# Optimization experiments

Hardware: AMD Instinct MI355X
Metric: run time of the kernel (lower is better)

Reference implementation:

```python
import jax, jax.numpy as jnp
import numpy as np

B, N, D, H, K, FFN = 8, 256, 512, 16, 4, 2048
DK = D // H
NEG = -1e12


def _lin(k, i, o):
    return jax.random.normal(k, (i, o), jnp.float32) / np.sqrt(i)


def setup_inputs() -> dict:
    key = jax.random.key(0)
    ks = jax.random.split(key, 12)
    return {
        "x": jax.random.normal(ks[0], (B, N, D), jnp.float32),
        "dist": jax.random.uniform(ks[1], (B, N - 1, N - 1), jnp.float32) * 10.0,
        "dist_bar": jnp.array([1.5, 3.0, 5.0, 8.0], jnp.float32),
        "attn_bias": 0.1 * jax.random.normal(ks[2], (B, K, N, N), jnp.float32),
        "mask": jnp.ones((B, 1, N, N), jnp.int32),
        "num_heads": H,
        "Wq": _lin(ks[3], D, D), "bq": jnp.zeros((D,), jnp.float32),
        "Wk": _lin(ks[4], D, D), "bk": jnp.zeros((D,), jnp.float32),
        "Wv": _lin(ks[5], D, D), "bv": jnp.zeros((D,), jnp.float32),
        "W1": _lin(ks[6], K * D, D), "b1": jnp.zeros((D,), jnp.float32),
        "W2": _lin(ks[7], D, D), "b2": jnp.zeros((D,), jnp.float32),
        "g1": jnp.ones((D,), jnp.float32), "be1": jnp.zeros((D,), jnp.float32),
        "Wf1": _lin(ks[8], D, FFN), "bf1": jnp.zeros((FFN,), jnp.float32),
        "Wf2": _lin(ks[9], FFN, D), "bf2": jnp.zeros((D,), jnp.float32),
        "g2": jnp.ones((D,), jnp.float32), "be2": jnp.zeros((D,), jnp.float32),
    }


def _ln(x, g, b, eps=1e-6):
    m = jnp.mean(x, -1, keepdims=True)
    v = jnp.mean((x - m) ** 2, -1, keepdims=True)
    return (x - m) / jnp.sqrt(v + eps) * g + b


def _forward(x, dist, dist_bar, attn_bias, mask, num_heads,
             Wq, bq, Wk, bk, Wv, bv, W1, b1, W2, b2, g1, be1,
             Wf1, bf1, Wf2, bf2, g2, be2):
    Bn, Nn, Dn = x.shape
    Hh = num_heads
    dk = Dn // Hh
    Kk = dist_bar.shape[0]

    q = (x @ Wq + bq).reshape(Bn, Nn, Hh, dk).transpose(0, 2, 1, 3)  # [B,H,N,dk]
    k = (x @ Wk + bk).reshape(Bn, Nn, Hh, dk).transpose(0, 2, 1, 3)
    v = (x @ Wv + bv).reshape(Bn, Nn, Hh, dk).transpose(0, 2, 1, 3)

    scores = jnp.einsum('bhnd,bhmd->bhnm', q, k) / np.sqrt(dk)      # [B,H,N,N]
    # expand over scales and add bias: [B,H,K,N,N]
    scores = scores[:, :, None, :, :] + attn_bias[:, None, :, :, :]
    # padding mask [B,1,N,N] -> broadcast over H,K
    scores = jnp.where(mask[:, None] == 0, NEG, scores)

    # build padded distance with super node (row/col 0 distance = 0)
    nd = jnp.ones((Bn, Nn, Nn), x.dtype)
    nd = nd.at[:, 1:, 1:].set(dist)
    nd = nd.at[:, 0, :].set(0.0).at[:, :, 0].set(0.0)
    masks = nd[:, None, None, :, :] < dist_bar.reshape(1, 1, Kk, 1, 1)  # [B,1,K,N,N]
    masks = masks.at[:, :, :, 0, :].set(True).at[:, :, :, :, 0].set(True)

    scores = jnp.where(masks, scores, NEG)
    attn = jax.nn.softmax(scores, axis=-1)                           # [B,H,K,N,N]

    msg = jnp.einsum('bhknm,bhmd->bhknd', attn, v)                   # [B,H,K,N,dk]
    # faithful to torch: transpose(1,2).view(B,H*K,N,dk) then transpose(2,3).view(B,N,-1)
    msg = jnp.transpose(msg, (0, 2, 1, 3, 4)).reshape(Bn, Kk * Hh, Nn, dk)
    msg = jnp.transpose(msg, (0, 1, 3, 2)).reshape(Bn, Nn, Kk * Hh * dk)

    h = jax.nn.silu(msg @ W1 + b1) @ W2 + b2
    y = _ln(h + x, g1, be1)

    f = jax.nn.gelu(y @ Wf1 + bf1, approximate=False) @ Wf2 + bf2
    out = _ln(f + y, g2, be2)
    return out


def reference(x, dist, dist_bar, attn_bias, mask, num_heads,
              Wq, bq, Wk, bk, Wv, bv, W1, b1, W2, b2, g1, be1,
              Wf1, bf1, Wf2, bf2, g2, be2):
    return _forward(x, dist, dist_bar, attn_bias, mask, num_heads,
                    Wq, bq, Wk, bk, Wv, bv, W1, b1, W2, b2, g1, be1,
                    Wf1, bf1, Wf2, bf2, g2, be2)
```

## Files before the change

### kernel.cpp

```cpp
#include <hip/hip_runtime.h>
#include <math.h>

#define BB 8
#define NN 256
#define DD 512
#define HH 16
#define KK 4
#define DKK 32
#define FFN_ 2048
#define NEGV -1e12f

typedef __attribute__((ext_vector_type(8))) short bf16x8;
typedef __attribute__((ext_vector_type(4))) float f32x4;

__device__ __forceinline__ unsigned short f2bf(float f) {
    union { float f; unsigned int u; } v; v.f = f;
    unsigned int r = (v.u + 0x7FFFu + ((v.u >> 16) & 1u)) >> 16;
    return (unsigned short)r;
}
__device__ __forceinline__ float bf2f(unsigned short u) {
    union { unsigned int i; float f; } v; v.i = ((unsigned int)u) << 16;
    return v.f;
}
__device__ __forceinline__ void gload_lds16(const unsigned short* g, unsigned short* l) {
    __builtin_amdgcn_global_load_lds(
        (const __attribute__((address_space(1))) void*)g,
        (__attribute__((address_space(3))) void*)l, 16, 0, 0);
}

__global__ __launch_bounds__(256) void prep_kernel(
    const float* __restrict__ x,
    const float* __restrict__ Wq, const float* __restrict__ Wk,
    const float* __restrict__ Wv, const float* __restrict__ W1,
    const float* __restrict__ W2, const float* __restrict__ Wf1,
    const float* __restrict__ Wf2,
    const float* __restrict__ bq, const float* __restrict__ bk,
    const float* __restrict__ bv,
    const float* __restrict__ attn_bias, const int* __restrict__ mask,
    const float* __restrict__ dist, const float* __restrict__ dist_bar,
    unsigned short* __restrict__ xb, unsigned short* __restrict__ Wqkvt,
    unsigned short* __restrict__ W1t, unsigned short* __restrict__ W2t,
    unsigned short* __restrict__ Wf1t, unsigned short* __restrict__ Wf2t,
    float* __restrict__ bqkv, unsigned short* __restrict__ biasMs)
{
    const int z = blockIdx.z;
    const int t = threadIdx.x;

    if (z == 7) {
        if (blockIdx.x >= 1024) return;
        const int i0 = blockIdx.x * 1024 + t * 4;
        float4 xv = *(const float4*)(x + i0);
        ushort4 o;
        o.x = f2bf(xv.x); o.y = f2bf(xv.y); o.z = f2bf(xv.z); o.w = f2bf(xv.w);
        *(ushort4*)(xb + i0) = o;
        return;
    }
    if (z == 8) {
        if (blockIdx.x >= 6) return;
        const int i = blockIdx.x * 256 + t;
        float v = (i < 512) ? bq[i] : (i < 1024) ? bk[i - 512] : bv[i - 1024];
        bqkv[i] = v;
        return;
    }
    if (z == 9) {
        const int bx = blockIdx.x;
        const int rg = bx & 63, ks = (bx >> 6) & 3, b = bx >> 8;
        const int m = t;
        const float bar = dist_bar[ks];
        ushort4 o; unsigned short* po = (unsigned short*)&o;
        #pragma unroll
        for (int i = 0; i < 4; ++i) {
            const int n = rg * 4 + i;
            const int mk = mask[((size_t)(b * NN) + n) * NN + m];
            bool allowed = (n == 0) || (m == 0);
            if (!allowed)
                allowed = dist[((size_t)(b * 255) + (n - 1)) * 255 + (m - 1)] < bar;
            const float bias = attn_bias[(((size_t)(b * KK) + ks) * NN + n) * NN + m];
            po[i] = f2bf((mk != 0 && allowed) ? bias : NEGV);
        }
        *(ushort4*)(biasMs + (size_t)bx * 1024 + m * 4) = o;
        return;
    }

    const float* src; unsigned short* dst; int Kd, Nd;
    switch (z) {
        case 0: src = Wq;  dst = Wqkvt;              Kd = 512;  Nd = 512;  break;
        case 1: src = Wk;  dst = Wqkvt + 512 * 512;  Kd = 512;  Nd = 512;  break;
        case 2: src = Wv;  dst = Wqkvt + 1024 * 512; Kd = 512;  Nd = 512;  break;
        case 3: src = W1;  dst = W1t;  Kd = 2048; Nd = 512;  break;
        case 4: src = W2;  dst = W2t;  Kd = 512;  Nd = 512;  break;
        case 5: src = Wf1; dst = Wf1t; Kd = 512;  Nd = 2048; break;
        default: src = Wf2; dst = Wf2t; Kd = 2048; Nd = 512; break;
    }
    const int ktiles = Kd / 32, ntiles = Nd / 32;
    const int ti = blockIdx.x;
    if (ti >= ktiles * ntiles) return;
    const int k0 = (ti % ktiles) * 32, n0 = (ti / ktiles) * 32;

    __shared__ float tile[32][33];
    const int xx = t & 31, yy = t >> 5;
    #pragma unroll
    for (int r = 0; r < 4; ++r)
        tile[yy * 4 + r][xx] = src[(size_t)(k0 + yy * 4 + r) * Nd + n0 + xx];
    __syncthreads();
    #pragma unroll
    for (int r = 0; r < 4; ++r)
        dst[(size_t)(n0 + yy * 4 + r) * Kd + k0 + xx] = f2bf(tile[xx][yy * 4 + r]);
}

template<int ACT, int EPI>
__global__ __launch_bounds__(512) void mfma_gemm512(
    const unsigned short* __restrict__ A, const unsigned short* __restrict__ Bt,
    const float* __restrict__ bias, unsigned short* __restrict__ Cb,
    unsigned short* __restrict__ vT, int M, int N, int Kdim)
{
    __shared__ unsigned short As[128 * 64];
    __shared__ unsigned short Bs[128 * 64];

    const int t = threadIdx.x, lane = t & 63, wv = t >> 6;
    const int n0 = blockIdx.x * 128, m0 = blockIdx.y * 128;
    const int wm = wv >> 1, wn = wv & 1;
    const int L = lane & 15, qd = lane >> 4;
    const int sr = lane >> 3, sc = lane & 7;

    f32x4 acc[2][4];
    #pragma unroll
    for (int i = 0; i < 2; ++i)
        #pragma unroll
        for (int j = 0; j < 4; ++j) acc[i][j] = (f32x4){0.f, 0.f, 0.f, 0.f};

    for (int kt = 0; kt < Kdim; kt += 64) {
        #pragma unroll
        for (int p = 0; p < 2; ++p) {
            const int rbase = wv * 16 + p * 8;
            gload_lds16(A  + (size_t)(m0 + rbase + sr) * Kdim + kt + sc * 8,
                        As + rbase * 64);
            gload_lds16(Bt + (size_t)(n0 + rbase + sr) * Kdim + kt + sc * 8,
                        Bs + rbase * 64);
        }
        __syncthreads();
        #pragma unroll
        for (int s = 0; s < 2; ++s) {
            bf16x8 af[2], bfb[4];
            #pragma unroll
            for (int i = 0; i < 2; ++i)
                af[i] = *(const bf16x8*)(As + (wm * 32 + i * 16 + L) * 64 + s * 32 + qd * 8);
            #pragma unroll
            for (int j = 0; j < 4; ++j)
                bfb[j] = *(const bf16x8*)(Bs + (wn * 64 + j * 16 + L) * 64 + s * 32 + qd * 8);
            #pragma unroll
            for (int i = 0; i < 2; ++i)
                #pragma unroll
                for (int j = 0; j < 4; ++j)
                    acc[i][j] = __builtin_amdgcn_mfma_f32_16x16x32_bf16(af[i], bfb[j], acc[i][j], 0, 0, 0);
        }
        __syncthreads();
    }

    #pragma unroll
    for (int j = 0; j < 4; ++j) {
        const int col = n0 + wn * 64 + j * 16 + L;
        const float bv = bias[col];
        #pragma unroll
        for (int i = 0; i < 2; ++i) {
            const int rowb = m0 + wm * 32 + i * 16 + qd * 4;
            if (EPI == 1 && col >= 1024) {
                ushort4 pk; unsigned short* pp = (unsigned short*)&pk;
                #pragma unroll
                for (int r = 0; r < 4; ++r) pp[r] = f2bf(acc[i][j][r] + bv);
                *(ushort4*)(vT + (size_t)(col - 1024) * 2048 + rowb) = pk;
            } else {
                #pragma unroll
                for (int r = 0; r < 4; ++r) {
                    float v = acc[i][j][r] + bv;
                    if (ACT == 2) v = 0.5f * v * (1.0f + erff(v * 0.70710678118654752f));
                    Cb[(size_t)(rowb + r) * N + col] = f2bf(v);
                }
            }
        }
    }
}

template<int ACT>
__global__ __launch_bounds__(256) void mfma_gemm64(
    const unsigned short* __restrict__ A, const unsigned short* __restrict__ Bt,
    const float* __restrict__ bias, unsigned short* __restrict__ Cb,
    int M, int N, int Kdim)
{
    __shared__ unsigned short As[64 * 64];
    __shared__ unsigned short Bs[64 * 64];

    const int t = threadIdx.x, lane = t & 63, wv = t >> 6;
    const int n0 = blockIdx.x * 64, m0 = blockIdx.y * 64;
    const int r8 = lane >> 3, c8 = lane & 7;
    const int L = lane & 15, qd = lane >> 4;

    f32x4 acc[4];
    #pragma unroll
    for (int j = 0; j < 4; ++j) acc[j] = (f32x4){0.f, 0.f, 0.f, 0.f};

    for (int kt = 0; kt < Kdim; kt += 64) {
        #pragma unroll
        for (int i = 0; i < 2; ++i) {
            const int rbase = wv * 16 + i * 8;
            gload_lds16(A  + (size_t)(m0 + rbase + r8) * Kdim + kt + c8 * 8, As + rbase * 64);
            gload_lds16(Bt + (size_t)(n0 + rbase + r8) * Kdim + kt + c8 * 8, Bs + rbase * 64);
        }
        __syncthreads();
        #pragma unroll
        for (int s = 0; s < 2; ++s) {
            const bf16x8 a = *(const bf16x8*)(As + (wv * 16 + L) * 64 + s * 32 + qd * 8);
            #pragma unroll
            for (int j = 0; j < 4; ++j) {
                const bf16x8 b = *(const bf16x8*)(Bs + (j * 16 + L) * 64 + s * 32 + qd * 8);
                acc[j] = __builtin_amdgcn_mfma_f32_16x16x32_bf16(a, b, acc[j], 0, 0, 0);
            }
        }
        __syncthreads();
    }

    #pragma unroll
    for (int j = 0; j < 4; ++j) {
        const int col = n0 + j * 16 + L;
        const float bv = bias[col];
        #pragma unroll
        for (int r = 0; r < 4; ++r) {
            const int row = m0 + wv * 16 + qd * 4 + r;
            float v = acc[j][r] + bv;
            if (ACT == 1) v = v / (1.0f + __expf(-v));
            Cb[(size_t)row * N + col] = f2bf(v);
        }
    }
}

template<int KD, int OUT16>
__global__ __launch_bounds__(256) void gemm_ln(
    const unsigned short* __restrict__ A, const unsigned short* __restrict__ Bt,
    const float* __restrict__ bias, const float* __restrict__ res,
    const float* __restrict__ g, const float* __restrict__ be,
    float* __restrict__ out, unsigned short* __restrict__ outb)
{
    __shared__ unsigned short As[16 * 64];
    __shared__ unsigned short Bs[512 * 64];
    __shared__ float red1[4][16];
    __shared__ float red2[4][16];

    const int t = threadIdx.x, lane = t & 63, wv = t >> 6;
    const int L = lane & 15, qd = lane >> 4;
    const int m0 = blockIdx.x * 16;

    f32x4 acc[8];
    #pragma unroll
    for (int j = 0; j < 8; ++j) acc[j] = (f32x4){0.f, 0.f, 0.f, 0.f};

    for (int kt = 0; kt < KD; kt += 64) {
        if (t < 128)
            gload_lds16(A + (size_t)(m0 + (t >> 3)) * KD + kt + (t & 7) * 8,
                        As + (t >> 3) * 64);
        #pragma unroll
        for (int i = 0; i < 16; ++i)
            gload_lds16(Bt + (size_t)(i * 32 + (t >> 3)) * KD + kt + (t & 7) * 8,
                        Bs + (i * 32 + (t >> 3)) * 64);
        __syncthreads();
        #pragma unroll
        for (int s = 0; s < 2; ++s) {
            const bf16x8 a = *(const bf16x8*)(As + L * 64 + s * 32 + qd * 8);
            #pragma unroll
            for (int j = 0; j < 8; ++j) {
                const bf16x8 b = *(const bf16x8*)(Bs + (wv * 128 + j * 16 + L) * 64 + s * 32 + qd * 8);
                acc[j] = __builtin_amdgcn_mfma_f32_16x16x32_bf16(a, b, acc[j], 0, 0, 0);
            }
        }
        __syncthreads();
    }

    float val[8][4];
    #pragma unroll
    for (int j = 0; j < 8; ++j) {
        const int col = wv * 128 + j * 16 + L;
        const float bv = bias[col];
        #pragma unroll
        for (int r = 0; r < 4; ++r) {
            const int row = m0 + qd * 4 + r;
            val[j][r] = acc[j][r] + bv + res[(size_t)row * DD + col];
        }
    }

    float s[4] = {0.f, 0.f, 0.f, 0.f};
    #pragma unroll
    for (int j = 0; j < 8; ++j)
        #pragma unroll
        for (int r = 0; r < 4; ++r) s[r] += val[j][r];
    #pragma unroll
    for (int off = 8; off > 0; off >>= 1)
        #pragma unroll
        for (int r = 0; r < 4; ++r) s[r] += __shfl_xor(s[r], off);
    if (L == 0) {
        #pragma unroll
        for (int r = 0; r < 4; ++r) red1[wv][qd * 4 + r] = s[r];
    }
    __syncthreads();
    float mean[4];
    #pragma unroll
    for (int r = 0; r < 4; ++r) {
        const int rr = qd * 4 + r;
        mean[r] = (red1[0][rr] + red1[1][rr] + red1[2][rr] + red1[3][rr]) * (1.0f / 512.0f);
    }

    float v2[4] = {0.f, 0.f, 0.f, 0.f};
    #pragma unroll
    for (int j = 0; j < 8; ++j)
        #pragma unroll
        for (int r = 0; r < 4; ++r) {
            const float d = val[j][r] - mean[r];
            val[j][r] = d;
            v2[r] += d * d;
        }
    #pragma unroll
    for (int off = 8; off > 0; off >>= 1)
        #pragma unroll
        for (int r = 0; r < 4; ++r) v2[r] += __shfl_xor(v2[r], off);
    if (L == 0) {
        #pragma unroll
        for (int r = 0; r < 4; ++r) red2[wv][qd * 4 + r] = v2[r];
    }
    __syncthreads();
    float inv[4];
    #pragma unroll
    for (int r = 0; r < 4; ++r) {
        const int rr = qd * 4 + r;
        const float var = (red2[0][rr] + red2[1][rr] + red2[2][rr] + red2[3][rr]) * (1.0f / 512.0f);
        inv[r] = rsqrtf(var + 1e-6f);
    }

    #pragma unroll
    for (int j = 0; j < 8; ++j) {
        const int col = wv * 128 + j * 16 + L;
        const float gc = g[col], bc = be[col];
        #pragma unroll
        for (int r = 0; r < 4; ++r) {
            const int row = m0 + qd * 4 + r;
            const float o = val[j][r] * inv[r] * gc + bc;
            out[(size_t)row * DD + col] = o;
            if (OUT16) outb[(size_t)row * DD + col] = f2bf(o);
        }
    }
}

__global__ __launch_bounds__(256) void attn_kernel(
    const unsigned short* __restrict__ qkvb, const unsigned short* __restrict__ vT,
    const unsigned short* __restrict__ biasMs, unsigned short* __restrict__ msgT)
{
    const int qt = blockIdx.x, h = blockIdx.y, b = blockIdx.z;
    const int q0 = qt * 64;
    const int t = threadIdx.x, lane = t & 63, wv = t >> 6;
    const int L = lane & 15, qd = lane >> 4;

    __shared__ unsigned short Qs[64 * 32];
    __shared__ unsigned short Ks[256 * 32];
    __shared__ unsigned short Vs[32 * 264];
    __shared__ unsigned short Ps[64 * 264];
    __shared__ unsigned short Ot[32 * 72];

    {
        const int r = lane >> 2, c = lane & 3;
        gload_lds16(qkvb + (size_t)(b * NN + q0 + wv * 16 + r) * 1536 + h * DKK + c * 8,
                    Qs + wv * 16 * 32);
        #pragma unroll
        for (int p = 0; p < 4; ++p)
            gload_lds16(qkvb + (size_t)(b * NN + p * 64 + wv * 16 + r) * 1536 + 512 + h * DKK + c * 8,
                        Ks + (p * 64 + wv * 16) * 32);
    }
    {
        const int vr = t >> 3, seg = t & 7;
        const unsigned short* gv = vT + (size_t)(h * DKK + vr) * 2048 + b * NN + seg * 32;
        #pragma unroll
        for (int i = 0; i < 4; ++i) {
            bf16x8 vv = *(const bf16x8*)(gv + i * 8);
            *(bf16x8*)(Vs + vr * 264 + seg * 32 + i * 8) = vv;
        }
    }
    __syncthreads();

    f32x4 S[16];
    #pragma unroll
    for (int j = 0; j < 16; ++j) S[j] = (f32x4){0.f, 0.f, 0.f, 0.f};
    {
        const bf16x8 aq = *(const bf16x8*)(Qs + (wv * 16 + L) * 32 + qd * 8);
        #pragma unroll
        for (int j = 0; j < 16; ++j) {
            const bf16x8 bk = *(const bf16x8*)(Ks + (j * 16 + L) * 32 + qd * 8);
            S[j] = __builtin_amdgcn_mfma_f32_16x16x32_bf16(aq, bk, S[j], 0, 0, 0);
        }
    }
    const float scale = 0.17677669529663687f;
    const int rgb = (q0 + wv * 16) >> 2;

    for (int ks = 0; ks < KK; ++ks) {
        const unsigned short* bp = biasMs + ((size_t)((b * KK + ks) * 64 + rgb + qd)) * 1024;

        ushort4 b4[16];
        float mx[4] = {-3e38f, -3e38f, -3e38f, -3e38f};
        #pragma unroll
        for (int j = 0; j < 16; ++j) {
            b4[j] = *(const ushort4*)(bp + (j * 16 + L) * 4);
            const unsigned short* pb = (const unsigned short*)&b4[j];
            #pragma unroll
            for (int r = 0; r < 4; ++r)
                mx[r] = fmaxf(mx[r], S[j][r] * scale + bf2f(pb[r]));
        }
        #pragma unroll
        for (int off = 8; off > 0; off >>= 1)
            #pragma unroll
            for (int r = 0; r < 4; ++r) mx[r] = fmaxf(mx[r], __shfl_xor(mx[r], off));

        float sm[4] = {0.f, 0.f, 0.f, 0.f};
        #pragma unroll
        for (int j = 0; j < 16; ++j) {
            const unsigned short* pb = (const unsigned short*)&b4[j];
            #pragma unroll
            for (int r = 0; r < 4; ++r) {
                const float e = __expf(S[j][r] * scale + bf2f(pb[r]) - mx[r]);
                sm[r] += e;
                Ps[(wv * 16 + qd * 4 + r) * 264 + j * 16 + L] = f2bf(e);
            }
        }
        #pragma unroll
        for (int off = 8; off > 0; off >>= 1)
            #pragma unroll
            for (int r = 0; r < 4; ++r) sm[r] += __shfl_xor(sm[r], off);
        float inv[4];
        #pragma unroll
        for (int r = 0; r < 4; ++r) inv[r] = 1.0f / sm[r];

        f32x4 O[2];
        O[0] = (f32x4){0.f, 0.f, 0.f, 0.f};
        O[1] = (f32x4){0.f, 0.f, 0.f, 0.f};
        #pragma unroll
        for (int kc = 0; kc < 8; ++kc) {
            const bf16x8 ap = *(const bf16x8*)(Ps + (wv * 16 + L) * 264 + kc * 32 + qd * 8);
            #pragma unroll
            for (int jt = 0; jt < 2; ++jt) {
                const bf16x8 bv = *(const bf16x8*)(Vs + (jt * 16 + L) * 264 + kc * 32 + qd * 8);
                O[jt] = __builtin_amdgcn_mfma_f32_16x16x32_bf16(ap, bv, O[jt], 0, 0, 0);
            }
        }
        #pragma unroll
        for (int jt = 0; jt < 2; ++jt)
            #pragma unroll
            for (int r = 0; r < 4; ++r)
                Ot[(jt * 16 + L) * 72 + wv * 16 + qd * 4 + r] = f2bf(O[jt][r] * inv[r]);
        __syncthreads();

        {
            const int dd = t >> 3, cc = t & 7;
            bf16x8 ov = *(const bf16x8*)(Ot + dd * 72 + cc * 8);
            *(bf16x8*)(msgT + (size_t)b * 524288 +
                       ((size_t)((ks * HH + h) * DKK + dd)) * NN + q0 + cc * 8) = ov;
        }
        __syncthreads();
    }
}

extern "C" void kernel_launch(void* const* d_in, const int* in_sizes, int n_in,
                              void* d_out, int out_size, void* d_ws, size_t ws_size,
                              hipStream_t stream)
{
    const float* x         = (const float*)d_in[0];
    const float* dist      = (const float*)d_in[1];
    const float* dist_bar  = (const float*)d_in[2];
    const float* attn_bias = (const float*)d_in[3];
    const int*   mask      = (const int*)d_in[4];
    const float* Wq  = (const float*)d_in[6];  const float* bq  = (const float*)d_in[7];
    const float* Wk  = (const float*)d_in[8];  const float* bk  = (const float*)d_in[9];
    const float* Wv  = (const float*)d_in[10]; const float* bv  = (const float*)d_in[11];
    const float* W1  = (const float*)d_in[12]; const float* b1  = (const float*)d_in[13];
    const float* W2  = (const float*)d_in[14]; const float* b2  = (const float*)d_in[15];
    const float* g1  = (const float*)d_in[16]; const float* be1 = (const float*)d_in[17];
    const float* Wf1 = (const float*)d_in[18]; const float* bf1 = (const float*)d_in[19];
    const float* Wf2 = (const float*)d_in[20]; const float* bf2 = (const float*)d_in[21];
    const float* g2  = (const float*)d_in[22]; const float* be2 = (const float*)d_in[23];

    float* ws = (float*)d_ws;
    unsigned short* qkvb   = (unsigned short*)(ws + 0);
    unsigned short* vT     = (unsigned short*)(ws + 1572864);
    unsigned short* xb     = (unsigned short*)(ws + 2097152);
    unsigned short* msgT   = (unsigned short*)(ws + 2621440);
    unsigned short* g3     = msgT;
    unsigned short* biasMs = (unsigned short*)(ws + 4718592);
    float*          bqkv   = ws + 5767168;
    unsigned short* h1     = (unsigned short*)(ws + 5771264);
    float*          yb     = ws + 6295552;
    unsigned short* yb16   = (unsigned short*)(ws + 7344128);
    unsigned short* Wqkvt  = (unsigned short*)(ws + 7868416);
    unsigned short* W1t    = (unsigned short*)(ws + 8261632);
    unsigned short* W2t    = (unsigned short*)(ws + 8785920);
    unsigned short* Wf1t   = (unsigned short*)(ws + 8916992);
    unsigned short* Wf2t   = (unsigned short*)(ws + 9441280);
    float*          outp   = (float*)d_out;

    const int M = BB * NN;

    prep_kernel<<<dim3(2048, 1, 10), dim3(256), 0, stream>>>(
        x, Wq, Wk, Wv, W1, W2, Wf1, Wf2, bq, bk, bv,
        attn_bias, mask, dist, dist_bar,
        xb, Wqkvt, W1t, W2t, Wf1t, Wf2t, bqkv, biasMs);

    mfma_gemm512<0, 1><<<dim3(12, 16), dim3(512), 0, stream>>>(
        xb, Wqkvt, bqkv, qkvb, vT, M, 1536, DD);

    attn_kernel<<<dim3(4, HH, BB), dim3(256), 0, stream>>>(qkvb, vT, biasMs, msgT);

    mfma_gemm64<1><<<dim3(8, 32), dim3(256), 0, stream>>>(msgT, W1t, b1, h1, M, DD, 2048);

    gemm_ln<512, 1><<<dim3(128), dim3(256), 0, stream>>>(
        h1, W2t, b2, x, g1, be1, yb, yb16);

    mfma_gemm512<2, 0><<<dim3(16, 16), dim3(512), 0, stream>>>(
        yb16, Wf1t, bf1, g3, nullptr, M, FFN_, DD);

    gemm_ln<2048, 0><<<dim3(128), dim3(256), 0, stream>>>(
        g3, Wf2t, bf2, yb, g2, be2, outp, nullptr);
}
```

Baseline: 283.5 us.

## Unfuse GEMM+LayerNorm into 64x64-tile GEMMs plus standalone row LayerNorm kernels

```diff
diff --git a/kernel.cpp b/kernel.cpp
--- a/kernel.cpp
+++ b/kernel.cpp
@@ -181,11 +181,11 @@
     }
 }
 
-template<int ACT>
+template<int ACT, int OUTF32>
 __global__ __launch_bounds__(256) void mfma_gemm64(
     const unsigned short* __restrict__ A, const unsigned short* __restrict__ Bt,
     const float* __restrict__ bias, unsigned short* __restrict__ Cb,
-    int M, int N, int Kdim)
+    float* __restrict__ Cf, int M, int N, int Kdim)
 {
     __shared__ unsigned short As[64 * 64];
     __shared__ unsigned short Bs[64 * 64];
@@ -228,123 +228,44 @@
             const int row = m0 + wv * 16 + qd * 4 + r;
             float v = acc[j][r] + bv;
             if (ACT == 1) v = v / (1.0f + __expf(-v));
-            Cb[(size_t)row * N + col] = f2bf(v);
-        }
-    }
-}
-
-template<int KD, int OUT16>
-__global__ __launch_bounds__(256) void gemm_ln(
-    const unsigned short* __restrict__ A, const unsigned short* __restrict__ Bt,
-    const float* __restrict__ bias, const float* __restrict__ res,
+            if (OUTF32) Cf[(size_t)row * N + col] = v;
+            else        Cb[(size_t)row * N + col] = f2bf(v);
+        }
+    }
+}
+
+template<int OUT16>
+__global__ __launch_bounds__(256) void ln_kernel(
+    const float* __restrict__ a, const float* __restrict__ r,
     const float* __restrict__ g, const float* __restrict__ be,
     float* __restrict__ out, unsigned short* __restrict__ outb)
 {
-    __shared__ unsigned short As[16 * 64];
-    __shared__ unsigned short Bs[512 * 64];
-    __shared__ float red1[4][16];
-    __shared__ float red2[4][16];
-
     const int t = threadIdx.x, lane = t & 63, wv = t >> 6;
-    const int L = lane & 15, qd = lane >> 4;
-    const int m0 = blockIdx.x * 16;
-
-    f32x4 acc[8];
-    #pragma unroll
-    for (int j = 0; j < 8; ++j) acc[j] = (f32x4){0.f, 0.f, 0.f, 0.f};
-
-    for (int kt = 0; kt < KD; kt += 64) {
-        if (t < 128)
-            gload_lds16(A + (size_t)(m0 + (t >> 3)) * KD + kt + (t & 7) * 8,
-                        As + (t >> 3) * 64);
-        #pragma unroll
-        for (int i = 0; i < 16; ++i)
-            gload_lds16(Bt + (size_t)(i * 32 + (t >> 3)) * KD + kt + (t & 7) * 8,
-                        Bs + (i * 32 + (t >> 3)) * 64);
-        __syncthreads();
-        #pragma unroll
-        for (int s = 0; s < 2; ++s) {
-            const bf16x8 a = *(const bf16x8*)(As + L * 64 + s * 32 + qd * 8);
-            #pragma unroll
-            for (int j = 0; j < 8; ++j) {
-                const bf16x8 b = *(const bf16x8*)(Bs + (wv * 128 + j * 16 + L) * 64 + s * 32 + qd * 8);
-                acc[j] = __builtin_amdgcn_mfma_f32_16x16x32_bf16(a, b, acc[j], 0, 0, 0);
-            }
-        }
-        __syncthreads();
-    }
-
-    float val[8][4];
-    #pragma unroll
-    for (int j = 0; j < 8; ++j) {
-        const int col = wv * 128 + j * 16 + L;
-        const float bv = bias[col];
-        #pragma unroll
-        for (int r = 0; r < 4; ++r) {
-            const int row = m0 + qd * 4 + r;
-            val[j][r] = acc[j][r] + bv + res[(size_t)row * DD + col];
-        }
-    }
-
-    float s[4] = {0.f, 0.f, 0.f, 0.f};
-    #pragma unroll
-    for (int j = 0; j < 8; ++j)
-        #pragma unroll
-        for (int r = 0; r < 4; ++r) s[r] += val[j][r];
-    #pragma unroll
-    for (int off = 8; off > 0; off >>= 1)
-        #pragma unroll
-        for (int r = 0; r < 4; ++r) s[r] += __shfl_xor(s[r], off);
-    if (L == 0) {
-        #pragma unroll
-        for (int r = 0; r < 4; ++r) red1[wv][qd * 4 + r] = s[r];
-    }
-    __syncthreads();
-    float mean[4];
-    #pragma unroll
-    for (int r = 0; r < 4; ++r) {
-        const int rr = qd * 4 + r;
-        mean[r] = (red1[0][rr] + red1[1][rr] + red1[2][rr] + red1[3][rr]) * (1.0f / 512.0f);
-    }
-
-    float v2[4] = {0.f, 0.f, 0.f, 0.f};
-    #pragma unroll
-    for (int j = 0; j < 8; ++j)
-        #pragma unroll
-        for (int r = 0; r < 4; ++r) {
-            const float d = val[j][r] - mean[r];
-            val[j][r] = d;
-            v2[r] += d * d;
-        }
-    #pragma unroll
-    for (int off = 8; off > 0; off >>= 1)
-        #pragma unroll
-        for (int r = 0; r < 4; ++r) v2[r] += __shfl_xor(v2[r], off);
-    if (L == 0) {
-        #pragma unroll
-        for (int r = 0; r < 4; ++r) red2[wv][qd * 4 + r] = v2[r];
-    }
-    __syncthreads();
-    float inv[4];
-    #pragma unroll
-    for (int r = 0; r < 4; ++r) {
-        const int rr = qd * 4 + r;
-        const float var = (red2[0][rr] + red2[1][rr] + red2[2][rr] + red2[3][rr]) * (1.0f / 512.0f);
-        inv[r] = rsqrtf(var + 1e-6f);
-    }
-
-    #pragma unroll
-    for (int j = 0; j < 8; ++j) {
-        const int col = wv * 128 + j * 16 + L;
-        const float gc = g[col], bc = be[col];
-        #pragma unroll
-        for (int r = 0; r < 4; ++r) {
-            const int row = m0 + qd * 4 + r;
-            const float o = val[j][r] * inv[r] * gc + bc;
-            out[(size_t)row * DD + col] = o;
-            if (OUT16) outb[(size_t)row * DD + col] = f2bf(o);
-        }
-    }
+    const int row = blockIdx.x * 4 + wv;
+    const size_t base = (size_t)row * DD + lane * 8;
+    const int c0 = lane * 8;
+
+    float z[8]; float s = 0.f;
+    #pragma unroll
+    for (int i = 0; i < 8; ++i) { z[i] = a[base + i] + r[base + i]; s += z[i]; }
+    #pragma unroll
+    for (int off = 32; off > 0; off >>= 1) s += __shfl_xor(s, off);
+    const float mean = s * (1.0f / 512.0f);
+    float v = 0.f;
+    #pragma unroll
+    for (int i = 0; i < 8; ++i) { z[i] -= mean; v += z[i] * z[i]; }
+    #pragma unroll
+    for (int off = 32; off > 0; off >>= 1) v += __shfl_xor(v, off);
+    const float inv = rsqrtf(v * (1.0f / 512.0f) + 1e-6f);
+
+    unsigned short o16[8];
+    #pragma unroll
+    for (int i = 0; i < 8; ++i) {
+        const float o = z[i] * inv * g[c0 + i] + be[c0 + i];
+        out[base + i] = o;
+        if (OUT16) o16[i] = f2bf(o);
+    }
+    if (OUT16) *(bf16x8*)(outb + base) = *(bf16x8*)o16;
 }
 
 __global__ __launch_bounds__(256) void attn_kernel(
@@ -497,6 +418,8 @@
     unsigned short* W2t    = (unsigned short*)(ws + 8785920);
     unsigned short* Wf1t   = (unsigned short*)(ws + 8916992);
     unsigned short* Wf2t   = (unsigned short*)(ws + 9441280);
+    float*          h2     = ws + 9965568;
+    float*          fb     = ws + 11014144;
     float*          outp   = (float*)d_out;
 
     const int M = BB * NN;
@@ -511,14 +434,19 @@
 
     attn_kernel<<<dim3(4, HH, BB), dim3(256), 0, stream>>>(qkvb, vT, biasMs, msgT);
 
-    mfma_gemm64<1><<<dim3(8, 32), dim3(256), 0, stream>>>(msgT, W1t, b1, h1, M, DD, 2048);
-
-    gemm_ln<512, 1><<<dim3(128), dim3(256), 0, stream>>>(
-        h1, W2t, b2, x, g1, be1, yb, yb16);
+    mfma_gemm64<1, 0><<<dim3(8, 32), dim3(256), 0, stream>>>(
+        msgT, W1t, b1, h1, nullptr, M, DD, 2048);
+
+    mfma_gemm64<0, 1><<<dim3(8, 32), dim3(256), 0, stream>>>(
+        h1, W2t, b2, nullptr, h2, M, DD, DD);
+
+    ln_kernel<1><<<dim3(512), dim3(256), 0, stream>>>(h2, x, g1, be1, yb, yb16);
 
     mfma_gemm512<2, 0><<<dim3(16, 16), dim3(512), 0, stream>>>(
         yb16, Wf1t, bf1, g3, nullptr, M, FFN_, DD);
 
-    gemm_ln<2048, 0><<<dim3(128), dim3(256), 0, stream>>>(
-        g3, Wf2t, bf2, yb, g2, be2, outp, nullptr);
-}
+    mfma_gemm64<0, 1><<<dim3(8, 32), dim3(256), 0, stream>>>(
+        g3, Wf2t, bf2, nullptr, fb, M, DD, 2048);
+
+    ln_kernel<0><<<dim3(512), dim3(256), 0, stream>>>(fb, yb, g2, be2, outp, nullptr);
+}
```

Result: faster. 263.0 us (-7.2%).
